# Kernel optimization log

Hardware: AMD Instinct MI355X
Metric: run time of the kernel (lower is better)

Reference implementation:

```python
import jax, jax.numpy as jnp
import numpy as np

# static config (matches torch module instantiation)
B, D, NH, HD = 2, 256, 8, 32
NL, NP, DFF = 1, 4, 1024
SHAPES = [(180, 180)]          # (H, W) per level; 180*180 = 32400
STARTS = [0]
LSRC = 32400
N_DET, N_SEG = 200, 100        # SEG_QUERY_NUM=100 -> num_seg_query=300
LQ = N_DET + N_SEG


def _lin(key, dout, din, scale=None):
    scale = scale if scale is not None else 1.0 / np.sqrt(din)
    k1, k2 = jax.random.split(key)
    return (jax.random.normal(k1, (dout, din), jnp.float32) * scale,
            jax.random.normal(k2, (dout,), jnp.float32) * 0.01)


def setup_inputs() -> dict:
    key = jax.random.key(0)
    ks = iter(jax.random.split(key, 64))
    inp = {
        'query': jax.random.normal(next(ks), (B, LQ, D), jnp.float32),
        'query_pos': jax.random.normal(next(ks), (B, LQ, D), jnp.float32),
        'src': jax.random.normal(next(ks), (B, LSRC, D), jnp.float32),
        'pos': jax.random.normal(next(ks), (B, LSRC, D), jnp.float32),
        'reference_points': jax.random.uniform(next(ks), (B, LSRC + LQ, NL, 2), jnp.float32),
        'spatial_shapes': jnp.array(SHAPES, jnp.int32),
        'level_start_index': jnp.array(STARTS, jnp.int32),
    }
    # two MSDeformAttn instances (self_attn = sa_*, cross_attn = ca_*)
    for pre in ('sa', 'ca'):
        inp[pre + '_Wv'], inp[pre + '_bv'] = _lin(next(ks), D, D)
        inp[pre + '_Woff'], inp[pre + '_boff'] = _lin(next(ks), NH * NL * NP * 2, D, scale=0.01)
        inp[pre + '_Waw'], inp[pre + '_baw'] = _lin(next(ks), NH * NL * NP, D, scale=0.01)
        inp[pre + '_Wout'], inp[pre + '_bout'] = _lin(next(ks), D, D)
    for nm in ('norm1', 'norm2', 'normq', 'qa_norm', 'norm3'):
        inp[nm + '_g'] = jnp.ones((D,), jnp.float32)
        inp[nm + '_b'] = jnp.zeros((D,), jnp.float32)
    inp['ffn1_W1'], inp['ffn1_b1'] = _lin(next(ks), DFF, D)
    inp['ffn1_W2'], inp['ffn1_b2'] = _lin(next(ks), D, DFF)
    inp['ffn3_W1'], inp['ffn3_b1'] = _lin(next(ks), DFF, D)
    inp['ffn3_W2'], inp['ffn3_b2'] = _lin(next(ks), D, DFF)
    # TCSLayer: proj(d->2d) then gate1/gate2 (d->d), sigmoid gates
    inp['tcs_Wp'], inp['tcs_bp'] = _lin(next(ks), 2 * D, D)
    inp['tcs_Wg1'], inp['tcs_bg1'] = _lin(next(ks), D, D)
    inp['tcs_Wg2'], inp['tcs_bg2'] = _lin(next(ks), D, D)
    # query self-attention (nn.MultiheadAttention): packed in_proj [3D, D]
    inp['qa_Win'], inp['qa_bin'] = _lin(next(ks), 3 * D, D)
    inp['qa_Wout'], inp['qa_bout'] = _lin(next(ks), D, D)
    return inp


def ln(x, g, b, eps=1e-5):
    m = x.mean(-1, keepdims=True)
    v = ((x - m) ** 2).mean(-1, keepdims=True)
    return (x - m) * jax.lax.rsqrt(v + eps) * g + b


def msda(q, ref, src_v, Wv, bv, Woff, boff, Waw, baw, Wout, bout):
    """MSDeformAttn: value proj -> learned offsets/weights -> bilinear sample -> out proj.
    q [B,Lq,D], ref [B,Lq,NL,2] in [0,1], src_v [B,Lin,D]."""
    Bq, Lq, _ = q.shape
    Lin = src_v.shape[1]
    value = (src_v @ Wv.T + bv).reshape(Bq, Lin, NH, HD).transpose(0, 2, 1, 3)  # [B,NH,Lin,HD]
    off = (q @ Woff.T + boff).reshape(Bq, Lq, NH, NL, NP, 2)
    aw = jax.nn.softmax((q @ Waw.T + baw).reshape(Bq, Lq, NH, NL * NP), -1)
    aw = aw.reshape(Bq, Lq, NH, NL, NP)
    norm = jnp.array([[w, h] for (h, w) in SHAPES], q.dtype)  # [NL,2] = (W,H)
    loc = ref[:, :, None, :, None, :] + off / norm[None, None, None, :, None, :]
    out = jnp.zeros((Bq, NH, Lq, HD), q.dtype)
    for l, (h, w) in enumerate(SHAPES):
        s = STARTS[l]
        v_l = value[:, :, s:s + h * w, :]
        # grid_sample align_corners=False: pixel = loc*size - 0.5, zero padding
        x = loc[:, :, :, l, :, 0] * w - 0.5  # [B,Lq,NH,NP]
        y = loc[:, :, :, l, :, 1] * h - 0.5
        x0 = jnp.floor(x); y0 = jnp.floor(y)
        lx = x - x0; ly = y - y0
        x0i = x0.astype(jnp.int32); y0i = y0.astype(jnp.int32)
        samp = jnp.zeros((Bq, NH, Lq, NP, HD), q.dtype)
        for dy, dx, wgt in ((0, 0, (1 - lx) * (1 - ly)), (0, 1, lx * (1 - ly)),
                            (1, 0, (1 - lx) * ly), (1, 1, lx * ly)):
            xi = x0i + dx; yi = y0i + dy
            valid = ((xi >= 0) & (xi < w) & (yi >= 0) & (yi < h)).astype(q.dtype)
            idx = jnp.clip(yi, 0, h - 1) * w + jnp.clip(xi, 0, w - 1)  # [B,Lq,NH,NP]
            idx_t = idx.transpose(0, 2, 1, 3).reshape(Bq, NH, Lq * NP)
            g = jnp.take_along_axis(v_l, idx_t[..., None], axis=2).reshape(Bq, NH, Lq, NP, HD)
            samp = samp + g * (wgt * valid).transpose(0, 2, 1, 3)[..., None]
        out = out + jnp.einsum('bhqpd,bqhp->bhqd', samp, aw[:, :, :, l, :])
    out = out.transpose(0, 2, 1, 3).reshape(Bq, Lq, NH * HD)
    return out @ Wout.T + bout


def mha(x, pos, Win, bin_, Wout, bout):
    qk = x + pos
    q = (qk @ Win[:D].T + bin_[:D]).reshape(*x.shape[:2], NH, HD)
    k = (qk @ Win[D:2 * D].T + bin_[D:2 * D]).reshape(*x.shape[:2], NH, HD)
    v = (x @ Win[2 * D:].T + bin_[2 * D:]).reshape(*x.shape[:2], NH, HD)
    attn = jax.nn.softmax(jnp.einsum('bqhd,bkhd->bhqk', q, k) / np.sqrt(HD), -1)
    o = jnp.einsum('bhqk,bkhd->bqhd', attn, v).reshape(*x.shape[:2], D)
    return o @ Wout.T + bout


def reference(query, query_pos, src, pos, reference_points, spatial_shapes, level_start_index,
              sa_Wv, sa_bv, sa_Woff, sa_boff, sa_Waw, sa_baw, sa_Wout, sa_bout,
              ca_Wv, ca_bv, ca_Woff, ca_boff, ca_Waw, ca_baw, ca_Wout, ca_bout,
              norm1_g, norm1_b, norm2_g, norm2_b, normq_g, normq_b,
              qa_norm_g, qa_norm_b, norm3_g, norm3_b,
              ffn1_W1, ffn1_b1, ffn1_W2, ffn1_b2,
              ffn3_W1, ffn3_b1, ffn3_W2, ffn3_b2,
              tcs_Wp, tcs_bp, tcs_Wg1, tcs_bg1, tcs_Wg2, tcs_bg2,
              qa_Win, qa_bin, qa_Wout, qa_bout):
    # deformable self-attn over BEV tokens
    src2 = msda(src + pos, reference_points[:, :LSRC], src,
                sa_Wv, sa_bv, sa_Woff, sa_boff, sa_Waw, sa_baw, sa_Wout, sa_bout)
    src = ln(src + src2, norm1_g, norm1_b)
    # FFN 1
    h = jax.nn.relu(src @ ffn1_W1.T + ffn1_b1) @ ffn1_W2.T + ffn1_b2
    src = ln(src + h, norm2_g, norm2_b)
    # TCS gating (USE_SIGMOID_GATE, not SPLIT_GATE, no OCC)
    gd, gs = jnp.split(jax.nn.gelu(src @ tcs_Wp.T + tcs_bp, approximate=False), 2, axis=-1)
    gate_det = jax.nn.sigmoid(gd @ tcs_Wg1.T + tcs_bg1)
    gate_seg = jax.nn.sigmoid(gs @ tcs_Wg2.T + tcs_bg2)
    # gated deformable cross-attn (shared cross_attn weights)
    q_det = msda(query[:, :N_DET] + query_pos[:, :N_DET],
                 reference_points[:, LSRC:LSRC + N_DET], src * gate_det,
                 ca_Wv, ca_bv, ca_Woff, ca_boff, ca_Waw, ca_baw, ca_Wout, ca_bout)
    q_seg = msda(query[:, N_DET:LQ] + query_pos[:, N_DET:LQ],
                 reference_points[:, LSRC + N_DET:LSRC + LQ], src * gate_seg,
                 ca_Wv, ca_bv, ca_Woff, ca_boff, ca_Waw, ca_baw, ca_Wout, ca_bout)
    query2 = jnp.concatenate([q_det, q_seg], 1)
    query = ln(query + query2, normq_g, normq_b)
    # query self-attention (post-norm)
    query = ln(query + mha(query, query_pos, qa_Win, qa_bin, qa_Wout, qa_bout),
               qa_norm_g, qa_norm_b)
    # FFN 3
    h3 = jax.nn.relu(query @ ffn3_W1.T + ffn3_b1) @ ffn3_W2.T + ffn3_b2
    query = ln(query + h3, norm3_g, norm3_b)
    return (query, src, gate_det, gate_seg)
```

## Files before the change

kernel.cpp:

```cpp
#include <hip/hip_runtime.h>
#include <hip/hip_bf16.h>
#include <cmath>

using bf16 = __hip_bfloat16;
typedef __bf16 bf16x8 __attribute__((ext_vector_type(8)));
typedef __bf16 bf16x4 __attribute__((ext_vector_type(4)));
typedef float f32x4 __attribute__((ext_vector_type(4)));

constexpr int D = 256;
constexpr int LSRC = 32400;
constexpr int NB = 2;
constexpr int LQ = 300;
constexpr int NDET = 200;
constexpr int MS = NB * LSRC;
constexpr int MQ = NB * LQ;
constexpr int RP_STRIDE = LSRC + LQ;
constexpr float IMGW = 180.f, IMGH = 180.f;
constexpr int IW = 180, IH = 180;

constexpr long long OFF_Q  = 0;
constexpr long long OFF_S  = (long long)MQ * D;
constexpr long long OFF_GD = OFF_S + (long long)MS * D;
constexpr long long OFF_GS = OFF_GD + (long long)MS * D;

__device__ inline void gload16(const void* g, void* l) {
  __builtin_amdgcn_global_load_lds(
      (const __attribute__((address_space(1))) void*)g,
      (__attribute__((address_space(3))) void*)l, 16, 0, 0);
}

__device__ inline int xcd_swz(int b, int nwg) {
  int q = nwg >> 3, r = nwg & 7;
  int xcd = b & 7, i = b >> 3;
  return (xcd < r ? xcd * (q + 1) : r * (q + 1) + (xcd - r) * q) + i;
}

__global__ void detect_kernel(const void* g, int* flag) {
  *flag = (*(const unsigned*)g == 0x3F803F80u) ? 1 : 0;
}

struct CvtEnt { const void* src; void* dst; int n; int f32out; };
struct CvtBatch { CvtEnt e[48]; int blk0[49]; int cnt; };

__global__ __launch_bounds__(256) void cvt_batch_kernel(CvtBatch cb, const int* __restrict__ flag) {
  int bid = blockIdx.x;
  int i = 0;
  for (int j = 1; j < cb.cnt; ++j) if (cb.blk0[j] <= bid) i = j;
  const CvtEnt en = cb.e[i];
  int idx = (bid - cb.blk0[i]) * 2048 + threadIdx.x * 8;
  if (idx >= en.n) return;
  const bool isb = (*flag != 0);
  if (en.f32out) {
    float v[8];
    if (isb) {
      bf16x8 x = *(const bf16x8*)((const __bf16*)en.src + idx);
#pragma unroll
      for (int j = 0; j < 8; ++j) v[j] = (float)x[j];
    } else {
      const float* s = (const float*)en.src + idx;
#pragma unroll
      for (int j = 0; j < 8; ++j) v[j] = s[j];
    }
    float* o = (float*)en.dst + idx;
#pragma unroll
    for (int j = 0; j < 8; ++j) o[j] = v[j];
  } else {
    if (isb) {
      uint4 x = *(const uint4*)((const char*)en.src + (size_t)idx * 2);
      *(uint4*)((char*)en.dst + (size_t)idx * 2) = x;
    } else {
      const float* s = (const float*)en.src + idx;
      bf16x8 o;
#pragma unroll
      for (int j = 0; j < 8; ++j) o[j] = (__bf16)s[j];
      *(bf16x8*)((__bf16*)en.dst + idx) = o;
    }
  }
}

__global__ __launch_bounds__(256) void cvt_add(const void* __restrict__ a, const void* __restrict__ b,
                                               const int* __restrict__ flag,
                                               bf16* __restrict__ a_b, bf16* __restrict__ b_b,
                                               bf16* __restrict__ sum, int n8) {
  int i = blockIdx.x * 256 + threadIdx.x;
  if (i >= n8) return;
  const bool isb = (*flag != 0);
  float va[8], vb[8];
  bf16x8 ab, bb;
  if (isb) {
    ab = *(const bf16x8*)((const __bf16*)a + (size_t)i * 8);
    bb = *(const bf16x8*)((const __bf16*)b + (size_t)i * 8);
#pragma unroll
    for (int j = 0; j < 8; ++j) { va[j] = (float)ab[j]; vb[j] = (float)bb[j]; }
  } else {
    const float* pa = (const float*)a + (size_t)i * 8;
    const float* pb = (const float*)b + (size_t)i * 8;
#pragma unroll
    for (int j = 0; j < 8; ++j) { va[j] = pa[j]; vb[j] = pb[j]; ab[j] = (__bf16)va[j]; bb[j] = (__bf16)vb[j]; }
  }
  bf16x8 sb;
#pragma unroll
  for (int j = 0; j < 8; ++j) sb[j] = (__bf16)(va[j] + vb[j]);
  if (a_b) *(bf16x8*)((__bf16*)a_b + (size_t)i * 8) = ab;
  if (b_b) *(bf16x8*)((__bf16*)b_b + (size_t)i * 8) = bb;
  *(bf16x8*)((__bf16*)sum + (size_t)i * 8) = sb;
}

__global__ __launch_bounds__(256) void add8(const bf16* __restrict__ a, const bf16* __restrict__ b,
                                            bf16* __restrict__ o, int n8) {
  int i = blockIdx.x * 256 + threadIdx.x;
  if (i >= n8) return;
  bf16x8 va = *(const bf16x8*)((const __bf16*)a + (size_t)i * 8);
  bf16x8 vb = *(const bf16x8*)((const __bf16*)b + (size_t)i * 8);
  bf16x8 vo;
#pragma unroll
  for (int j = 0; j < 8; ++j) vo[j] = (__bf16)((float)va[j] + (float)vb[j]);
  *(bf16x8*)((__bf16*)o + (size_t)i * 8) = vo;
}

template<int ACT, int OUTB, int RESM>
__global__ __launch_bounds__(256) void gemm_bt(
    const bf16* __restrict__ A, int lda,
    const bf16* __restrict__ Wt,
    const bf16* __restrict__ bias,
    const void* __restrict__ res,
    void* __restrict__ out, int ldo,
    int M, int N, int K)
{
  __shared__ __bf16 As[2][64 * 32];
  __shared__ __bf16 Bs[2][64 * 32];
  const int gy = gridDim.y;
  const int nwg = gridDim.x * gy;
  const int t = xcd_swz(blockIdx.y * gridDim.x + blockIdx.x, nwg);
  const int m0 = (t / gy) * 64;
  const int n0 = (t % gy) * 64;
  const int tid = threadIdx.x;
  const int lane = tid & 63, wid = tid >> 6;
  const int wm = (wid >> 1) * 32, wn = (wid & 1) * 32;
  f32x4 acc[2][2] = {};
  const int lr = tid >> 2;
  const int lc = (tid & 3) * 8;
  const bf16* Ap = A + (size_t)(m0 + lr) * lda + lc;
  const bf16* Wp = Wt + (size_t)(n0 + lr) * K + lc;
  const int fr = lane & 15, ks = (lane >> 4) * 8;

  for (int k0 = 0; k0 < K; k0 += 64) {
    __syncthreads();
#pragma unroll
    for (int kk = 0; kk < 2; ++kk) {
      const int kc = k0 + kk * 32;
      gload16((const __bf16*)Ap + kc, &As[kk][8 * tid]);
      gload16((const __bf16*)Wp + kc, &Bs[kk][8 * tid]);
    }
    __syncthreads();
#pragma unroll
    for (int kk = 0; kk < 2; ++kk) {
      bf16x8 a0 = *(const bf16x8*)&As[kk][(wm + fr) * 32 + ks];
      bf16x8 a1 = *(const bf16x8*)&As[kk][(wm + 16 + fr) * 32 + ks];
      bf16x8 b0 = *(const bf16x8*)&Bs[kk][(wn + fr) * 32 + ks];
      bf16x8 b1 = *(const bf16x8*)&Bs[kk][(wn + 16 + fr) * 32 + ks];
      acc[0][0] = __builtin_amdgcn_mfma_f32_16x16x32_bf16(a0, b0, acc[0][0], 0, 0, 0);
      acc[0][1] = __builtin_amdgcn_mfma_f32_16x16x32_bf16(a0, b1, acc[0][1], 0, 0, 0);
      acc[1][0] = __builtin_amdgcn_mfma_f32_16x16x32_bf16(a1, b0, acc[1][0], 0, 0, 0);
      acc[1][1] = __builtin_amdgcn_mfma_f32_16x16x32_bf16(a1, b1, acc[1][1], 0, 0, 0);
    }
  }

  const int rq = (lane >> 4) * 4;
#pragma unroll
  for (int fm = 0; fm < 2; ++fm)
#pragma unroll
  for (int fn = 0; fn < 2; ++fn) {
    int ncol = n0 + wn + fn * 16 + fr;
    if (ncol >= N) continue;
    float bvs = (float)bias[ncol];
#pragma unroll
    for (int i = 0; i < 4; ++i) {
      int mrow = m0 + wm + fm * 16 + rq + i;
      if (mrow >= M) continue;
      float v = acc[fm][fn][i] + bvs;
      if (RESM == 1) v += (float)((const bf16*)res)[(size_t)mrow * ldo + ncol];
      else if (RESM == 2) v += ((const float*)res)[(size_t)mrow * ldo + ncol];
      if (ACT == 1) v = fmaxf(v, 0.f);
      else if (ACT == 2) v = 0.5f * v * (1.f + erff(v * 0.7071067811865476f));
      else if (ACT == 3) v = 1.f / (1.f + __expf(-v));
      if (OUTB) ((bf16*)out)[(size_t)mrow * ldo + ncol] = (bf16)v;
      else ((float*)out)[(size_t)mrow * ldo + ncol] = v;
    }
  }
}

template<int ACT, int OUTB, int RESM, int EMIT>
__global__ __launch_bounds__(256) void gemm128(
    const bf16* __restrict__ A, int lda,
    const bf16* __restrict__ Wt,
    const bf16* __restrict__ bias,
    const void* __restrict__ res,
    void* __restrict__ out, int ldo,
    int M, int N, int K,
    const int* __restrict__ flagp, void* __restrict__ ob, long long eoff)
{
  __shared__ __bf16 As[2][128 * 32];
  __shared__ __bf16 Bs[2][128 * 32];
  const int gy = gridDim.y;
  const int nwg = gridDim.x * gy;
  const int t = xcd_swz(blockIdx.y * gridDim.x + blockIdx.x, nwg);
  const int m0 = (t / gy) * 128;
  const int n0 = (t % gy) * 128;
  const int tid = threadIdx.x;
  const int lane = tid & 63, wid = tid >> 6;
  const int wr = (wid >> 1) * 64, wc = (wid & 1) * 64;
  const int fr = lane & 15, ks = (lane >> 4) * 8;
  f32x4 acc[4][4] = {};

  const int srow = tid >> 2;
  const int scol = (tid & 3) * 8;
  const bf16* Ap0 = A + (size_t)(m0 + srow) * lda + scol;
  const bf16* Ap1 = A + (size_t)(m0 + 64 + srow) * lda + scol;
  const bf16* Bp0 = Wt + (size_t)(n0 + srow) * K + scol;
  const bf16* Bp1 = Wt + (size_t)(n0 + 64 + srow) * K + scol;

  for (int k0 = 0; k0 < K; k0 += 64) {
    __syncthreads();
#pragma unroll
    for (int kk = 0; kk < 2; ++kk) {
      const int kc = k0 + kk * 32;
      gload16((const __bf16*)Ap0 + kc, &As[kk][8 * tid]);
      gload16((const __bf16*)Ap1 + kc, &As[kk][64 * 32 + 8 * tid]);
      gload16((const __bf16*)Bp0 + kc, &Bs[kk][8 * tid]);
      gload16((const __bf16*)Bp1 + kc, &Bs[kk][64 * 32 + 8 * tid]);
    }
    __syncthreads();
#pragma unroll
    for (int kk = 0; kk < 2; ++kk) {
      bf16x8 af[4], bfv[4];
#pragma unroll
      for (int m = 0; m < 4; ++m) af[m]  = *(const bf16x8*)&As[kk][(wr + m * 16 + fr) * 32 + ks];
#pragma unroll
      for (int n = 0; n < 4; ++n) bfv[n] = *(const bf16x8*)&Bs[kk][(wc + n * 16 + fr) * 32 + ks];
#pragma unroll
      for (int m = 0; m < 4; ++m)
#pragma unroll
        for (int n = 0; n < 4; ++n)
          acc[m][n] = __builtin_amdgcn_mfma_f32_16x16x32_bf16(af[m], bfv[n], acc[m][n], 0, 0, 0);
    }
  }

  const bool isb = EMIT ? (*flagp != 0) : false;
  const int rq = (lane >> 4) * 4;
#pragma unroll
  for (int m = 0; m < 4; ++m) {
    const int mb = m0 + wr + m * 16 + rq;
#pragma unroll
    for (int n = 0; n < 4; ++n) {
      const int ncol = n0 + wc + n * 16 + fr;
      const float bvs = (float)bias[ncol];
#pragma unroll
      for (int i = 0; i < 4; ++i) {
        const int mrow = mb + i;
        if (mrow >= M) continue;
        float v = acc[m][n][i] + bvs;
        if (RESM == 1) v += (float)((const bf16*)res)[(size_t)mrow * ldo + ncol];
        else if (RESM == 2) v += ((const float*)res)[(size_t)mrow * ldo + ncol];
        if (ACT == 1) v = fmaxf(v, 0.f);
        else if (ACT == 2) v = 0.5f * v * (1.f + erff(v * 0.7071067811865476f));
        else if (ACT == 3) v = 1.f / (1.f + __expf(-v));
        if (OUTB) ((bf16*)out)[(size_t)mrow * ldo + ncol] = (bf16)v;
        else ((float*)out)[(size_t)mrow * ldo + ncol] = v;
        if (EMIT) {
          long long eo = eoff + (long long)mrow * ldo + ncol;
          if (isb) ((__bf16*)ob)[eo] = (__bf16)v;
          else ((float*)ob)[eo] = v;
        }
      }
    }
  }
}

__global__ __launch_bounds__(256) void gemm_gated(
    const bf16* __restrict__ S, const bf16* __restrict__ G, int lda,
    const bf16* __restrict__ Wt,
    const bf16* __restrict__ bias,
    bf16* __restrict__ out, int ldo,
    int M, int N, int K)
{
  __shared__ __bf16 As[2][128 * 32];
  __shared__ __bf16 Bs[2][128 * 32];
  const int gy = gridDim.y;
  const int nwg = gridDim.x * gy;
  const int t = xcd_swz(blockIdx.y * gridDim.x + blockIdx.x, nwg);
  const int m0 = (t / gy) * 128;
  const int n0 = (t % gy) * 128;
  const int tid = threadIdx.x;
  const int lane = tid & 63, wid = tid >> 6;
  const int wr = (wid >> 1) * 64, wc = (wid & 1) * 64;
  const int fr = lane & 15, ks = (lane >> 4) * 8;
  f32x4 acc[4][4] = {};

  const int srow = tid >> 2;
  const int scol = (tid & 3) * 8;
  const bf16* Sp0 = S + (size_t)(m0 + srow) * lda + scol;
  const bf16* Sp1 = S + (size_t)(m0 + 64 + srow) * lda + scol;
  const bf16* Gp0 = G + (size_t)(m0 + srow) * lda + scol;
  const bf16* Gp1 = G + (size_t)(m0 + 64 + srow) * lda + scol;
  const bf16* Bp0 = Wt + (size_t)(n0 + srow) * K + scol;
  const bf16* Bp1 = Wt + (size_t)(n0 + 64 + srow) * K + scol;

  for (int k0 = 0; k0 < K; k0 += 64) {
    bf16x8 a0[2], a1[2];
#pragma unroll
    for (int kk = 0; kk < 2; ++kk) {
      const int kc = k0 + kk * 32;
      bf16x8 s0 = *(const bf16x8*)((const __bf16*)Sp0 + kc);
      bf16x8 g0 = *(const bf16x8*)((const __bf16*)Gp0 + kc);
      bf16x8 s1 = *(const bf16x8*)((const __bf16*)Sp1 + kc);
      bf16x8 g1 = *(const bf16x8*)((const __bf16*)Gp1 + kc);
#pragma unroll
      for (int j = 0; j < 8; ++j) {
        a0[kk][j] = (__bf16)((float)s0[j] * (float)g0[j]);
        a1[kk][j] = (__bf16)((float)s1[j] * (float)g1[j]);
      }
    }
    __syncthreads();
#pragma unroll
    for (int kk = 0; kk < 2; ++kk) {
      const int kc = k0 + kk * 32;
      *(bf16x8*)&As[kk][8 * tid] = a0[kk];
      *(bf16x8*)&As[kk][64 * 32 + 8 * tid] = a1[kk];
      gload16((const __bf16*)Bp0 + kc, &Bs[kk][8 * tid]);
      gload16((const __bf16*)Bp1 + kc, &Bs[kk][64 * 32 + 8 * tid]);
    }
    __syncthreads();
#pragma unroll
    for (int kk = 0; kk < 2; ++kk) {
      bf16x8 af[4], bfv[4];
#pragma unroll
      for (int m = 0; m < 4; ++m) af[m]  = *(const bf16x8*)&As[kk][(wr + m * 16 + fr) * 32 + ks];
#pragma unroll
      for (int n = 0; n < 4; ++n) bfv[n] = *(const bf16x8*)&Bs[kk][(wc + n * 16 + fr) * 32 + ks];
#pragma unroll
      for (int m = 0; m < 4; ++m)
#pragma unroll
        for (int n = 0; n < 4; ++n)
          acc[m][n] = __builtin_amdgcn_mfma_f32_16x16x32_bf16(af[m], bfv[n], acc[m][n], 0, 0, 0);
    }
  }

  const int rq = (lane >> 4) * 4;
#pragma unroll
  for (int m = 0; m < 4; ++m) {
    const int mb = m0 + wr + m * 16 + rq;
#pragma unroll
    for (int n = 0; n < 4; ++n) {
      const int ncol = n0 + wc + n * 16 + fr;
      const float bvs = (float)bias[ncol];
#pragma unroll
      for (int i = 0; i < 4; ++i) {
        const int mrow = mb + i;
        if (mrow >= M) continue;
        out[(size_t)mrow * ldo + ncol] = (bf16)(acc[m][n][i] + bvs);
      }
    }
  }
}

template<int RESM, int EMIT, int OUTF>
__global__ __launch_bounds__(256) void gemm_ln(
    const bf16* __restrict__ A, int lda,
    const bf16* __restrict__ Wt,
    const bf16* __restrict__ bias,
    const void* __restrict__ res,
    const bf16* __restrict__ g, const bf16* __restrict__ b,
    bf16* __restrict__ outb, float* __restrict__ outf,
    int M, int K,
    const int* __restrict__ flagp, void* __restrict__ ob, long long eoff)
{
  __shared__ __bf16 As[2][64 * 32];
  __shared__ __bf16 Bs[2][256 * 32];
  __shared__ float redS[4][64], redQ[4][64];
  const int m0 = blockIdx.x * 64;
  const int tid = threadIdx.x, lane = tid & 63, wid = tid >> 6;
  const int wc = wid * 64;
  const int fr = lane & 15, ks = (lane >> 4) * 8;
  f32x4 acc[4][4] = {};
  const int srow = tid >> 2, scol = (tid & 3) * 8;
  const bf16* Ap = A + (size_t)(m0 + srow) * lda + scol;
  const bf16* Bp = Wt + (size_t)srow * K + scol;

  for (int k0 = 0; k0 < K; k0 += 64) {
    __syncthreads();
#pragma unroll
    for (int kk = 0; kk < 2; ++kk) {
      const int kc = k0 + kk * 32;
      gload16((const __bf16*)Ap + kc, &As[kk][8 * tid]);
#pragma unroll
      for (int j = 0; j < 4; ++j)
        gload16((const __bf16*)(Bp + (size_t)j * 64 * K) + kc, &Bs[kk][j * 64 * 32 + 8 * tid]);
    }
    __syncthreads();
#pragma unroll
    for (int kk = 0; kk < 2; ++kk) {
      bf16x8 af[4], bfv[4];
#pragma unroll
      for (int m = 0; m < 4; ++m) af[m]  = *(const bf16x8*)&As[kk][(m * 16 + fr) * 32 + ks];
#pragma unroll
      for (int n = 0; n < 4; ++n) bfv[n] = *(const bf16x8*)&Bs[kk][(wc + n * 16 + fr) * 32 + ks];
#pragma unroll
      for (int m = 0; m < 4; ++m)
#pragma unroll
        for (int n = 0; n < 4; ++n)
          acc[m][n] = __builtin_amdgcn_mfma_f32_16x16x32_bf16(af[m], bfv[n], acc[m][n], 0, 0, 0);
    }
  }

  const int rq = (lane >> 4) * 4;
  float bvals[4], gvals[4], bb2[4];
#pragma unroll
  for (int n = 0; n < 4; ++n) {
    bvals[n] = (float)bias[wc + n * 16 + fr];
    gvals[n] = (float)g[wc + n * 16 + fr];
    bb2[n]   = (float)b[wc + n * 16 + fr];
  }
#pragma unroll
  for (int m = 0; m < 4; ++m)
#pragma unroll
  for (int i = 0; i < 4; ++i) {
    const int mrow = m0 + m * 16 + rq + i;
#pragma unroll
    for (int n = 0; n < 4; ++n) {
      float r;
      if (RESM == 1) r = (float)((const bf16*)res)[(size_t)mrow * 256 + wc + n * 16 + fr];
      else           r = ((const float*)res)[(size_t)mrow * 256 + wc + n * 16 + fr];
      acc[m][n][i] += bvals[n] + r;
    }
    float s = acc[m][0][i] + acc[m][1][i] + acc[m][2][i] + acc[m][3][i];
    float q = acc[m][0][i] * acc[m][0][i] + acc[m][1][i] * acc[m][1][i]
            + acc[m][2][i] * acc[m][2][i] + acc[m][3][i] * acc[m][3][i];
#pragma unroll
    for (int off = 1; off <= 8; off <<= 1) {
      s += __shfl_xor(s, off);
      q += __shfl_xor(q, off);
    }
    if (fr == 0) { redS[wid][m * 16 + rq + i] = s; redQ[wid][m * 16 + rq + i] = q; }
  }
  __syncthreads();
  const bool isb = EMIT ? (*flagp != 0) : false;
#pragma unroll
  for (int m = 0; m < 4; ++m)
#pragma unroll
  for (int i = 0; i < 4; ++i) {
    const int rl = m * 16 + rq + i;
    const int mrow = m0 + rl;
    if (mrow >= M) continue;
    float ts = redS[0][rl] + redS[1][rl] + redS[2][rl] + redS[3][rl];
    float tq = redQ[0][rl] + redQ[1][rl] + redQ[2][rl] + redQ[3][rl];
    float mean = ts * (1.f / 256.f);
    float var = tq * (1.f / 256.f) - mean * mean;
    float rstd = rsqrtf(var + 1e-5f);
#pragma unroll
    for (int n = 0; n < 4; ++n) {
      const int col = wc + n * 16 + fr;
      float y = (acc[m][n][i] - mean) * rstd * gvals[n] + bb2[n];
      if (outb) outb[(size_t)mrow * 256 + col] = (bf16)y;
      if (OUTF) outf[(size_t)mrow * 256 + col] = y;
      if (EMIT) {
        long long eo = eoff + (long long)mrow * 256 + col;
        if (isb) ((__bf16*)ob)[eo] = (__bf16)y;
        else ((float*)ob)[eo] = y;
      }
    }
  }
}

__global__ __launch_bounds__(256) void msda_sample4(
    const float* __restrict__ oa,
    const float* __restrict__ rpf, int rp_base, int qi0, int qcnt4, int lqrow,
    const bf16* __restrict__ val, bf16* __restrict__ out, int swz) {
  int blk = blockIdx.x;
  if (swz) blk = xcd_swz(blk, gridDim.x);
  int b = blk / qcnt4;
  int wid = threadIdx.x >> 6, lane = threadIdx.x & 63;
  int qi = qi0 + (blk % qcnt4) * 4 + wid;
  size_t row = (size_t)b * lqrow + qi;
  int h = lane >> 3, d0 = (lane & 7) * 4;
  const __bf16* vb = (const __bf16*)val + (size_t)b * LSRC * 256 + h * 32 + d0;
  float rx = rpf[((size_t)b * RP_STRIDE + rp_base + qi) * 2 + 0];
  float ry = rpf[((size_t)b * RP_STRIDE + rp_base + qi) * 2 + 1];
  const float* offp = oa + row * 96 + h * 8;
  const float* awp  = oa + row * 96 + 64 + h * 4;
  float a0 = awp[0], a1 = awp[1], a2 = awp[2], a3 = awp[3];
  float mx = fmaxf(fmaxf(a0, a1), fmaxf(a2, a3));
  float e0 = __expf(a0 - mx), e1 = __expf(a1 - mx), e2 = __expf(a2 - mx), e3 = __expf(a3 - mx);
  float rs = 1.f / (e0 + e1 + e2 + e3);
  float aws[4] = { e0 * rs, e1 * rs, e2 * rs, e3 * rs };
  float o0 = 0.f, o1 = 0.f, o2 = 0.f, o3 = 0.f;
#pragma unroll
  for (int p = 0; p < 4; ++p) {
    float x = rx * IMGW + offp[p * 2 + 0] - 0.5f;
    float y = ry * IMGH + offp[p * 2 + 1] - 0.5f;
    float x0f = floorf(x), y0f = floorf(y);
    float lx = x - x0f, ly = y - y0f;
    int x0 = (int)x0f, y0 = (int)y0f;
#pragma unroll
    for (int dy = 0; dy < 2; ++dy)
#pragma unroll
    for (int dx = 0; dx < 2; ++dx) {
      int xi = x0 + dx, yi = y0 + dy;
      if (xi >= 0 && xi < IW && yi >= 0 && yi < IH) {
        float wgt = aws[p] * (dx ? lx : 1.f - lx) * (dy ? ly : 1.f - ly);
        bf16x4 gv = *(const bf16x4*)(vb + (size_t)(yi * IW + xi) * 256);
        o0 += wgt * (float)gv[0]; o1 += wgt * (float)gv[1];
        o2 += wgt * (float)gv[2]; o3 += wgt * (float)gv[3];
      }
    }
  }
  bf16x4 ov;
  ov[0] = (__bf16)o0; ov[1] = (__bf16)o1; ov[2] = (__bf16)o2; ov[3] = (__bf16)o3;
  *(bf16x4*)((__bf16*)out + row * 256 + h * 32 + d0) = ov;
}

__global__ __launch_bounds__(256) void mha_attn(
    const float* __restrict__ qk,
    const float* __restrict__ v,
    bf16* __restrict__ o) {
  __shared__ float probs[4][304];
  int bh = blockIdx.x / 75;
  int j  = blockIdx.x % 75;
  int b = bh >> 3, h = bh & 7;
  int wid = threadIdx.x >> 6, lane = threadIdx.x & 63;
  const float scale = 0.17677669529663687f;
  int q = j * 4 + wid;
  const float* qv = qk + ((size_t)(b * 300 + q)) * 512 + h * 32;
  float p[5];
  float mx = -1e30f;
#pragma unroll
  for (int s5 = 0; s5 < 5; ++s5) {
    int k = lane + 64 * s5;
    float sacc = -1e30f;
    if (k < 300) {
      const float* kv = qk + ((size_t)(b * 300 + k)) * 512 + 256 + h * 32;
      float sd = 0.f;
#pragma unroll
      for (int dd = 0; dd < 32; ++dd) sd += qv[dd] * kv[dd];
      sacc = sd * scale;
    }
    p[s5] = sacc;
    mx = fmaxf(mx, sacc);
  }
#pragma unroll
  for (int off = 32; off; off >>= 1) mx = fmaxf(mx, __shfl_xor(mx, off));
  float ssum = 0.f;
#pragma unroll
  for (int s5 = 0; s5 < 5; ++s5) {
    p[s5] = (p[s5] > -1e29f) ? __expf(p[s5] - mx) : 0.f;
    ssum += p[s5];
  }
#pragma unroll
  for (int off = 32; off; off >>= 1) ssum += __shfl_xor(ssum, off);
  float rinv = 1.f / ssum;
#pragma unroll
  for (int s5 = 0; s5 < 5; ++s5) {
    int k = lane + 64 * s5;
    if (k < 300) probs[wid][k] = p[s5] * rinv;
  }
  __syncthreads();
  {
    int d = lane & 31, half = lane >> 5;
    float acc = 0.f;
    for (int k = half * 150; k < half * 150 + 150; ++k)
      acc += probs[wid][k] * v[((size_t)(b * 300 + k)) * 256 + h * 32 + d];
    acc += __shfl_xor(acc, 32);
    if (lane < 32) o[((size_t)(b * 300 + q)) * 256 + h * 32 + d] = (bf16)acc;
  }
}

extern "C" void kernel_launch(void* const* d_in, const int* in_sizes, int n_in,
                              void* d_out, int out_size, void* d_ws, size_t ws_size,
                              hipStream_t stream) {
  (void)n_in; (void)out_size; (void)ws_size;
  const size_t SZ = (size_t)MS * D * sizeof(bf16);

  char* w = (char*)d_ws;
  auto carve = [&](size_t bytes) { char* p = w; w += (bytes + 255) & ~(size_t)255; return p; };

  int*   flag = (int*)carve(256);
  float* rp_f = (float*)carve((size_t)NB * RP_STRIDE * 2 * 4);

  bf16* wb[51] = {};
  bf16* wcat_s = nullptr; bf16* bcat_s = nullptr;
  bf16* wcat_q = nullptr; bf16* bcat_q = nullptr;
  for (int i = 7; i <= 50; ++i) {
    if (i == 9)       { wcat_s = (bf16*)carve((size_t)96 * 256 * 2); wb[9]  = wcat_s; }
    else if (i == 10) { bcat_s = (bf16*)carve(96 * 2);               wb[10] = bcat_s; }
    else if (i == 11) { wb[11] = wcat_s + 64 * 256; }
    else if (i == 12) { wb[12] = bcat_s + 64; }
    else if (i == 17) { wcat_q = (bf16*)carve((size_t)96 * 256 * 2); wb[17] = wcat_q; }
    else if (i == 18) { bcat_q = (bf16*)carve(96 * 2);               wb[18] = bcat_q; }
    else if (i == 19) { wb[19] = wcat_q + 64 * 256; }
    else if (i == 20) { wb[20] = bcat_q + 64; }
    else wb[i] = (bf16*)carve((size_t)in_sizes[i] * 2);
  }

  bf16* query_b     = (bf16*)carve((size_t)MQ * D * 2);
  bf16* query_pos_b = (bf16*)carve((size_t)MQ * D * 2);
  bf16* qx_q        = (bf16*)carve((size_t)MQ * D * 2);
  bf16* att_q       = (bf16*)carve((size_t)MQ * D * 2);
  bf16* q_x         = (bf16*)carve((size_t)MQ * D * 2);
  bf16* qpx         = (bf16*)carve((size_t)MQ * D * 2);
  bf16* mha_o       = (bf16*)carve((size_t)MQ * D * 2);
  bf16* lnq_b       = (bf16*)carve((size_t)MQ * D * 2);
  bf16* qh          = (bf16*)carve((size_t)MQ * 1024 * 2);
  float* qoffawb    = (float*)carve((size_t)MQ * 96 * 4);
  float* q_res      = (float*)carve((size_t)MQ * D * 4);
  float* qk_f       = (float*)carve((size_t)MQ * 512 * 4);
  float* v_f        = (float*)carve((size_t)MQ * D * 4);

  char* A = carve(SZ);
  char* B = carve(SZ);
  char* C = carve(SZ);
  char* Dd = carve(SZ);
  char* E = carve(SZ);
  carve(512 * 1024);

  const bf16* query     = (const bf16*)d_in[0];
  const bf16* query_pos = (const bf16*)d_in[1];
  const bf16* src       = (const bf16*)d_in[2];
  const bf16* pos       = (const bf16*)d_in[3];

  dim3 blk(256);
  const int GS64  = (MS + 63) / 64;
  const int GQ64  = (MQ + 63) / 64;
  const int G128  = (MS + 127) / 128;
  const int G128h = (MS / 2 + 127) / 128;

  detect_kernel<<<1, 1, 0, stream>>>(d_in[23], flag);
  {
    CvtBatch cb{};
    int nb = 0, cnt = 0;
    auto addcvt = [&](const void* s, void* dst, int n, int f32o) {
      cb.e[cnt] = { s, dst, n, f32o };
      cb.blk0[cnt] = nb;
      nb += (n + 2047) / 2048;
      ++cnt;
    };
    addcvt(d_in[4], rp_f, in_sizes[4], 1);
    for (int i = 7; i <= 50; ++i) addcvt(d_in[i], wb[i], in_sizes[i], 0);
    cb.cnt = cnt;
    cvt_batch_kernel<<<nb, blk, 0, stream>>>(cb, flag);
  }
  bf16* src_b = (bf16*)A;
  bf16* qx    = (bf16*)C;
  cvt_add<<<MS * D / 8 / 256, blk, 0, stream>>>(src, pos, flag, src_b, nullptr, qx, MS * D / 8);
  cvt_add<<<MQ * D / 8 / 256, blk, 0, stream>>>(query, query_pos, flag, query_b, query_pos_b, qx_q, MQ * D / 8);

  float* offawb = (float*)B;
  bf16*  val    = (bf16*)Dd;
  gemm_bt<0,0,0><<<dim3(GS64,2), blk, 0, stream>>>(qx, 256, wb[9], wb[10], nullptr, offawb, 96, MS, 96, 256);
  gemm128<0,1,0,0><<<dim3(G128,2), blk, 0, stream>>>(src_b, 256, wb[7], wb[8], nullptr, val, 256, MS, 256, 256, nullptr, nullptr, 0);
  bf16* samp = (bf16*)C;
  msda_sample4<<<NB * (LSRC / 4), blk, 0, stream>>>(offawb, rp_f, 0, 0, LSRC / 4, LSRC, val, samp, 1);
  bf16* lnx = (bf16*)C;
  gemm_ln<1,0,0><<<GS64, blk, 0, stream>>>(samp, 256, wb[13], wb[14], src_b, wb[23], wb[24],
                                           lnx, nullptr, MS, 256, nullptr, nullptr, 0);

  bf16* srcout = (bf16*)A;
  {
    const int CH = MS / 2;
    const int GC128 = (CH + 127) / 128;
    const int GC64  = (CH + 63) / 64;
    bf16* hid = (bf16*)Dd;
    for (int c = 0; c < 2; ++c) {
      size_t ro = (size_t)c * CH * 256;
      gemm128<1,1,0,0><<<dim3(GC128,8), blk, 0, stream>>>(lnx + ro, 256, wb[33], wb[34], nullptr, hid, 1024, CH, 1024, 256, nullptr, nullptr, 0);
      gemm_ln<1,1,0><<<GC64, blk, 0, stream>>>(hid, 1024, wb[35], wb[36], lnx + ro, wb[25], wb[26],
                                               srcout + ro, nullptr, CH, 1024, flag, d_out, OFF_S + (long long)ro);
    }
  }

  bf16* gdt = (bf16*)B;
  bf16* gst = (bf16*)E;
  {
    const int CH = MS / 2;
    bf16* proj = (bf16*)C;
    for (int c = 0; c < 2; ++c) {
      size_t ro = (size_t)c * CH * 256;
      gemm128<2,1,0,0><<<dim3(G128h,4), blk, 0, stream>>>(srcout + ro, 256, wb[41], wb[42], nullptr, proj, 512, CH, 512, 256, nullptr, nullptr, 0);
      gemm128<3,1,0,1><<<dim3(G128h,2), blk, 0, stream>>>(proj,       512, wb[43], wb[44], nullptr, gdt + ro, 256, CH, 256, 256, flag, d_out, OFF_GD + (long long)ro);
      gemm128<3,1,0,1><<<dim3(G128h,2), blk, 0, stream>>>(proj + 256, 512, wb[45], wb[46], nullptr, gst + ro, 256, CH, 256, 256, flag, d_out, OFF_GS + (long long)ro);
    }
  }

  gemm_bt<0,0,0><<<dim3(GQ64,2), blk, 0, stream>>>(qx_q, 256, wb[17], wb[18], nullptr, qoffawb, 96, MQ, 96, 256);

  gemm_gated<<<dim3(G128,2), blk, 0, stream>>>(srcout, gdt, 256, wb[15], wb[16], val, 256, MS, 256, 256);
  msda_sample4<<<NB * (NDET / 4), blk, 0, stream>>>(qoffawb, rp_f, LSRC, 0, NDET / 4, LQ, val, att_q, 0);
  gemm_gated<<<dim3(G128,2), blk, 0, stream>>>(srcout, gst, 256, wb[15], wb[16], val, 256, MS, 256, 256);
  msda_sample4<<<NB * ((LQ - NDET) / 4), blk, 0, stream>>>(qoffawb, rp_f, LSRC, NDET, (LQ - NDET) / 4, LQ, val, att_q, 0);

  gemm_ln<1,0,1><<<GQ64, blk, 0, stream>>>(att_q, 256, wb[21], wb[22], query_b, wb[27], wb[28],
                                           q_x, q_res, MQ, 256, nullptr, nullptr, 0);

  add8<<<MQ * D / 8 / 256, blk, 0, stream>>>(q_x, query_pos_b, qpx, MQ * D / 8);
  gemm_bt<0,0,0><<<dim3(GQ64,8), blk, 0, stream>>>(qpx, 256, wb[47], wb[48], nullptr, qk_f, 512, MQ, 512, 256);
  gemm_bt<0,0,0><<<dim3(GQ64,4), blk, 0, stream>>>(q_x, 256, wb[47] + (size_t)512 * 256, wb[48] + 512, nullptr, v_f, 256, MQ, 256, 256);
  mha_attn<<<NB * 8 * 75, blk, 0, stream>>>(qk_f, v_f, mha_o);
  gemm_ln<2,0,1><<<GQ64, blk, 0, stream>>>(mha_o, 256, wb[49], wb[50], q_res, wb[29], wb[30],
                                           q_x, q_res, MQ, 256, nullptr, nullptr, 0);

  gemm_bt<1,1,0><<<dim3(GQ64,16), blk, 0, stream>>>(q_x, 256, wb[37], wb[38], nullptr, qh, 1024, MQ, 1024, 256);
  gemm_ln<2,1,0><<<GQ64, blk, 0, stream>>>(qh, 1024, wb[39], wb[40], q_res, wb[31], wb[32],
                                           lnq_b, nullptr, MQ, 1024, flag, d_out, OFF_Q);
}
```

Before: 759.2 us.

## Fuse input conversion and adds into GEMM loads, merge gated cross-attn passes

Removes the large src+pos convert/add pass and instead reads the raw inputs (fp32 or bf16) directly inside the offset/attention GEMM, value GEMM and residual of the LayerNorm GEMM. The two gated value projections now run as one launch over a z-dimension into separate buffers, so the det and seg sampling run as a single kernel. The gate projection loops are unchunked into full-size launches, and the query+pos add before the MHA projection is folded into the GEMM's A-load. This saves a full-size intermediate write and read and several launches, at the cost of extra buffer space and redundant fp32 loads, since both GEMMs now read src separately.

```diff
diff --git a/kernel.cpp b/kernel.cpp
--- a/kernel.cpp
+++ b/kernel.cpp
@@ -33,6 +33,31 @@
   int q = nwg >> 3, r = nwg & 7;
   int xcd = b & 7, i = b >> 3;
   return (xcd < r ? xcd * (q + 1) : r * (q + 1) + (xcd - r) * q) + i;
+}
+
+__device__ inline bf16x8 ld8_dyn(const void* p, size_t off, bool isb) {
+  if (isb) return *(const bf16x8*)((const __bf16*)p + off);
+  bf16x8 r;
+  const float* f = (const float*)p + off;
+#pragma unroll
+  for (int j = 0; j < 8; ++j) r[j] = (__bf16)f[j];
+  return r;
+}
+
+__device__ inline bf16x8 ld8_add_dyn(const void* a, const void* b, size_t off, bool isb) {
+  bf16x8 r;
+  if (isb) {
+    bf16x8 x = *(const bf16x8*)((const __bf16*)a + off);
+    bf16x8 y = *(const bf16x8*)((const __bf16*)b + off);
+#pragma unroll
+    for (int j = 0; j < 8; ++j) r[j] = (__bf16)((float)x[j] + (float)y[j]);
+  } else {
+    const float* fa = (const float*)a + off;
+    const float* fb = (const float*)b + off;
+#pragma unroll
+    for (int j = 0; j < 8; ++j) r[j] = (__bf16)(fa[j] + fb[j]);
+  }
+  return r;
 }
 
 __global__ void detect_kernel(const void* g, int* flag) {
@@ -104,18 +129,6 @@
   if (a_b) *(bf16x8*)((__bf16*)a_b + (size_t)i * 8) = ab;
   if (b_b) *(bf16x8*)((__bf16*)b_b + (size_t)i * 8) = bb;
   *(bf16x8*)((__bf16*)sum + (size_t)i * 8) = sb;
-}
-
-__global__ __launch_bounds__(256) void add8(const bf16* __restrict__ a, const bf16* __restrict__ b,
-                                            bf16* __restrict__ o, int n8) {
-  int i = blockIdx.x * 256 + threadIdx.x;
-  if (i >= n8) return;
-  bf16x8 va = *(const bf16x8*)((const __bf16*)a + (size_t)i * 8);
-  bf16x8 vb = *(const bf16x8*)((const __bf16*)b + (size_t)i * 8);
-  bf16x8 vo;
-#pragma unroll
-  for (int j = 0; j < 8; ++j) vo[j] = (__bf16)((float)va[j] + (float)vb[j]);
-  *(bf16x8*)((__bf16*)o + (size_t)i * 8) = vo;
 }
 
 template<int ACT, int OUTB, int RESM>
@@ -190,6 +203,74 @@
   }
 }
 
+template<int ADYN>
+__global__ __launch_bounds__(256) void gemm_bt_add(
+    const void* __restrict__ A1, const void* __restrict__ A2, int lda,
+    const bf16* __restrict__ Wt, const bf16* __restrict__ bias,
+    float* __restrict__ out, int ldo, int M, int N, int K,
+    const int* __restrict__ flagp)
+{
+  __shared__ __bf16 As[2][64 * 32];
+  __shared__ __bf16 Bs[2][64 * 32];
+  const int gy = gridDim.y;
+  const int nwg = gridDim.x * gy;
+  const int t = xcd_swz(blockIdx.y * gridDim.x + blockIdx.x, nwg);
+  const int m0 = (t / gy) * 64;
+  const int n0 = (t % gy) * 64;
+  const int tid = threadIdx.x;
+  const int lane = tid & 63, wid = tid >> 6;
+  const int wm = (wid >> 1) * 32, wn = (wid & 1) * 32;
+  f32x4 acc[2][2] = {};
+  const int lr = tid >> 2;
+  const int lc = (tid & 3) * 8;
+  const int ar = min(m0 + lr, M - 1);
+  const size_t abase = (size_t)ar * lda + lc;
+  const bf16* Wp = Wt + (size_t)(n0 + lr) * K + lc;
+  const bool isb = ADYN ? (*flagp != 0) : true;
+  const int fr = lane & 15, ks = (lane >> 4) * 8;
+
+  for (int k0 = 0; k0 < K; k0 += 64) {
+    bf16x8 av[2];
+#pragma unroll
+    for (int kk = 0; kk < 2; ++kk)
+      av[kk] = ld8_add_dyn(A1, A2, abase + k0 + kk * 32, isb);
+    __syncthreads();
+#pragma unroll
+    for (int kk = 0; kk < 2; ++kk) {
+      *(bf16x8*)&As[kk][8 * tid] = av[kk];
+      gload16((const __bf16*)Wp + k0 + kk * 32, &Bs[kk][8 * tid]);
+    }
+    __syncthreads();
+#pragma unroll
+    for (int kk = 0; kk < 2; ++kk) {
+      bf16x8 a0 = *(const bf16x8*)&As[kk][(wm + fr) * 32 + ks];
+      bf16x8 a1 = *(const bf16x8*)&As[kk][(wm + 16 + fr) * 32 + ks];
+      bf16x8 b0 = *(const bf16x8*)&Bs[kk][(wn + fr) * 32 + ks];
+      bf16x8 b1 = *(const bf16x8*)&Bs[kk][(wn + 16 + fr) * 32 + ks];
+      acc[0][0] = __builtin_amdgcn_mfma_f32_16x16x32_bf16(a0, b0, acc[0][0], 0, 0, 0);
+      acc[0][1] = __builtin_amdgcn_mfma_f32_16x16x32_bf16(a0, b1, acc[0][1], 0, 0, 0);
+      acc[1][0] = __builtin_amdgcn_mfma_f32_16x16x32_bf16(a1, b0, acc[1][0], 0, 0, 0);
+      acc[1][1] = __builtin_amdgcn_mfma_f32_16x16x32_bf16(a1, b1, acc[1][1], 0, 0, 0);
+    }
+  }
+
+  const int rq = (lane >> 4) * 4;
+#pragma unroll
+  for (int fm = 0; fm < 2; ++fm)
+#pragma unroll
+  for (int fn = 0; fn < 2; ++fn) {
+    int ncol = n0 + wn + fn * 16 + fr;
+    if (ncol >= N) continue;
+    float bvs = (float)bias[ncol];
+#pragma unroll
+    for (int i = 0; i < 4; ++i) {
+      int mrow = m0 + wm + fm * 16 + rq + i;
+      if (mrow >= M) continue;
+      out[(size_t)mrow * ldo + ncol] = acc[fm][fn][i] + bvs;
+    }
+  }
+}
+
 template<int ACT, int OUTB, int RESM, int EMIT>
 __global__ __launch_bounds__(256) void gemm128(
     const bf16* __restrict__ A, int lda,
@@ -277,15 +358,18 @@
   }
 }
 
-__global__ __launch_bounds__(256) void gemm_gated(
-    const bf16* __restrict__ S, const bf16* __restrict__ G, int lda,
-    const bf16* __restrict__ Wt,
-    const bf16* __restrict__ bias,
-    bf16* __restrict__ out, int ldo,
-    int M, int N, int K)
+template<int OP, int SDYN>
+__global__ __launch_bounds__(256) void gemm128_rs(
+    const void* __restrict__ S, const bf16* __restrict__ G0, const bf16* __restrict__ G1,
+    int lda,
+    const bf16* __restrict__ Wt, const bf16* __restrict__ bias,
+    bf16* __restrict__ out0, bf16* __restrict__ out1, int ldo,
+    int M, int N, int K, const int* __restrict__ flagp)
 {
   __shared__ __bf16 As[2][128 * 32];
   __shared__ __bf16 Bs[2][128 * 32];
+  const bf16* G = blockIdx.z ? G1 : G0;
+  bf16* out = blockIdx.z ? out1 : out0;
   const int gy = gridDim.y;
   const int nwg = gridDim.x * gy;
   const int t = xcd_swz(blockIdx.y * gridDim.x + blockIdx.x, nwg);
@@ -299,32 +383,38 @@
 
   const int srow = tid >> 2;
   const int scol = (tid & 3) * 8;
-  const bf16* Sp0 = S + (size_t)(m0 + srow) * lda + scol;
-  const bf16* Sp1 = S + (size_t)(m0 + 64 + srow) * lda + scol;
-  const bf16* Gp0 = G + (size_t)(m0 + srow) * lda + scol;
-  const bf16* Gp1 = G + (size_t)(m0 + 64 + srow) * lda + scol;
+  const int r0 = min(m0 + srow, M - 1);
+  const int r1 = min(m0 + 64 + srow, M - 1);
+  const size_t s0off = (size_t)r0 * lda + scol;
+  const size_t s1off = (size_t)r1 * lda + scol;
   const bf16* Bp0 = Wt + (size_t)(n0 + srow) * K + scol;
   const bf16* Bp1 = Wt + (size_t)(n0 + 64 + srow) * K + scol;
+  const bool isb = SDYN ? (*flagp != 0) : true;
 
   for (int k0 = 0; k0 < K; k0 += 64) {
     bf16x8 a0[2], a1[2];
 #pragma unroll
     for (int kk = 0; kk < 2; ++kk) {
-      const int kc = k0 + kk * 32;
-      bf16x8 s0 = *(const bf16x8*)((const __bf16*)Sp0 + kc);
-      bf16x8 g0 = *(const bf16x8*)((const __bf16*)Gp0 + kc);
-      bf16x8 s1 = *(const bf16x8*)((const __bf16*)Sp1 + kc);
-      bf16x8 g1 = *(const bf16x8*)((const __bf16*)Gp1 + kc);
-#pragma unroll
-      for (int j = 0; j < 8; ++j) {
-        a0[kk][j] = (__bf16)((float)s0[j] * (float)g0[j]);
-        a1[kk][j] = (__bf16)((float)s1[j] * (float)g1[j]);
+      const int kc = kk * 32 + k0;
+      bf16x8 s0 = ld8_dyn(S, s0off + kc, isb);
+      bf16x8 s1 = ld8_dyn(S, s1off + kc, isb);
+      if (OP == 1) {
+        bf16x8 g0 = *(const bf16x8*)((const __bf16*)G + s0off + kc);
+        bf16x8 g1 = *(const bf16x8*)((const __bf16*)G + s1off + kc);
+#pragma unroll
+        for (int j = 0; j < 8; ++j) {
+          a0[kk][j] = (__bf16)((float)s0[j] * (float)g0[j]);
+          a1[kk][j] = (__bf16)((float)s1[j] * (float)g1[j]);
+        }
+      } else {
+        a0[kk] = s0;
+        a1[kk] = s1;
       }
     }
     __syncthreads();
 #pragma unroll
     for (int kk = 0; kk < 2; ++kk) {
-      const int kc = k0 + kk * 32;
+      const int kc = kk * 32 + k0;
       *(bf16x8*)&As[kk][8 * tid] = a0[kk];
       *(bf16x8*)&As[kk][64 * 32 + 8 * tid] = a1[kk];
       gload16((const __bf16*)Bp0 + kc, &Bs[kk][8 * tid]);
@@ -414,6 +504,7 @@
   }
 
   const int rq = (lane >> 4) * 4;
+  const bool fb = (EMIT || RESM == 3) ? (*flagp != 0) : false;
   float bvals[4], gvals[4], bb2[4];
 #pragma unroll
   for (int n = 0; n < 4; ++n) {
@@ -426,11 +517,14 @@
 #pragma unroll
   for (int i = 0; i < 4; ++i) {
     const int mrow = m0 + m * 16 + rq + i;
+    const int rr = mrow < M ? mrow : M - 1;
 #pragma unroll
     for (int n = 0; n < 4; ++n) {
+      const size_t ri = (size_t)rr * 256 + wc + n * 16 + fr;
       float r;
-      if (RESM == 1) r = (float)((const bf16*)res)[(size_t)mrow * 256 + wc + n * 16 + fr];
-      else           r = ((const float*)res)[(size_t)mrow * 256 + wc + n * 16 + fr];
+      if (RESM == 1) r = (float)((const bf16*)res)[ri];
+      else if (RESM == 2) r = ((const float*)res)[ri];
+      else r = fb ? (float)((const bf16*)res)[ri] : ((const float*)res)[ri];
       acc[m][n][i] += bvals[n] + r;
     }
     float s = acc[m][0][i] + acc[m][1][i] + acc[m][2][i] + acc[m][3][i];
@@ -444,7 +538,6 @@
     if (fr == 0) { redS[wid][m * 16 + rq + i] = s; redQ[wid][m * 16 + rq + i] = q; }
   }
   __syncthreads();
-  const bool isb = EMIT ? (*flagp != 0) : false;
 #pragma unroll
   for (int m = 0; m < 4; ++m)
 #pragma unroll
@@ -465,7 +558,7 @@
       if (OUTF) outf[(size_t)mrow * 256 + col] = y;
       if (EMIT) {
         long long eo = eoff + (long long)mrow * 256 + col;
-        if (isb) ((__bf16*)ob)[eo] = (__bf16)y;
+        if (fb) ((__bf16*)ob)[eo] = (__bf16)y;
         else ((float*)ob)[eo] = y;
       }
     }
@@ -474,15 +567,17 @@
 
 __global__ __launch_bounds__(256) void msda_sample4(
     const float* __restrict__ oa,
-    const float* __restrict__ rpf, int rp_base, int qi0, int qcnt4, int lqrow,
-    const bf16* __restrict__ val, bf16* __restrict__ out, int swz) {
+    const float* __restrict__ rpf, int rp_base, int qcnt4, int lqrow, int split,
+    const bf16* __restrict__ valA, const bf16* __restrict__ valB,
+    bf16* __restrict__ out, int swz) {
   int blk = blockIdx.x;
   if (swz) blk = xcd_swz(blk, gridDim.x);
   int b = blk / qcnt4;
   int wid = threadIdx.x >> 6, lane = threadIdx.x & 63;
-  int qi = qi0 + (blk % qcnt4) * 4 + wid;
+  int qi = (blk % qcnt4) * 4 + wid;
   size_t row = (size_t)b * lqrow + qi;
   int h = lane >> 3, d0 = (lane & 7) * 4;
+  const bf16* val = (qi < split) ? valA : valB;
   const __bf16* vb = (const __bf16*)val + (size_t)b * LSRC * 256 + h * 32 + d0;
   float rx = rpf[((size_t)b * RP_STRIDE + rp_base + qi) * 2 + 0];
   float ry = rpf[((size_t)b * RP_STRIDE + rp_base + qi) * 2 + 1];
@@ -606,7 +701,6 @@
   bf16* qx_q        = (bf16*)carve((size_t)MQ * D * 2);
   bf16* att_q       = (bf16*)carve((size_t)MQ * D * 2);
   bf16* q_x         = (bf16*)carve((size_t)MQ * D * 2);
-  bf16* qpx         = (bf16*)carve((size_t)MQ * D * 2);
   bf16* mha_o       = (bf16*)carve((size_t)MQ * D * 2);
   bf16* lnq_b       = (bf16*)carve((size_t)MQ * D * 2);
   bf16* qh          = (bf16*)carve((size_t)MQ * 1024 * 2);
@@ -624,14 +718,13 @@
 
   const bf16* query     = (const bf16*)d_in[0];
   const bf16* query_pos = (const bf16*)d_in[1];
-  const bf16* src       = (const bf16*)d_in[2];
-  const bf16* pos       = (const bf16*)d_in[3];
+  const void* src       = d_in[2];
+  const void* pos       = d_in[3];
 
   dim3 blk(256);
   const int GS64  = (MS + 63) / 64;
   const int GQ64  = (MQ + 63) / 64;
   const int G128  = (MS + 127) / 128;
-  const int G128h = (MS / 2 + 127) / 128;
 
   detect_kernel<<<1, 1, 0, stream>>>(d_in[23], flag);
   {
@@ -648,20 +741,17 @@
     cb.cnt = cnt;
     cvt_batch_kernel<<<nb, blk, 0, stream>>>(cb, flag);
   }
-  bf16* src_b = (bf16*)A;
-  bf16* qx    = (bf16*)C;
-  cvt_add<<<MS * D / 8 / 256, blk, 0, stream>>>(src, pos, flag, src_b, nullptr, qx, MS * D / 8);
   cvt_add<<<MQ * D / 8 / 256, blk, 0, stream>>>(query, query_pos, flag, query_b, query_pos_b, qx_q, MQ * D / 8);
 
   float* offawb = (float*)B;
   bf16*  val    = (bf16*)Dd;
-  gemm_bt<0,0,0><<<dim3(GS64,2), blk, 0, stream>>>(qx, 256, wb[9], wb[10], nullptr, offawb, 96, MS, 96, 256);
-  gemm128<0,1,0,0><<<dim3(G128,2), blk, 0, stream>>>(src_b, 256, wb[7], wb[8], nullptr, val, 256, MS, 256, 256, nullptr, nullptr, 0);
+  gemm_bt_add<1><<<dim3(GS64,2), blk, 0, stream>>>(src, pos, 256, wb[9], wb[10], offawb, 96, MS, 96, 256, flag);
+  gemm128_rs<0,1><<<dim3(G128,2,1), blk, 0, stream>>>(src, nullptr, nullptr, 256, wb[7], wb[8], val, nullptr, 256, MS, 256, 256, flag);
   bf16* samp = (bf16*)C;
-  msda_sample4<<<NB * (LSRC / 4), blk, 0, stream>>>(offawb, rp_f, 0, 0, LSRC / 4, LSRC, val, samp, 1);
+  msda_sample4<<<NB * (LSRC / 4), blk, 0, stream>>>(offawb, rp_f, 0, LSRC / 4, LSRC, 1 << 30, val, val, samp, 1);
   bf16* lnx = (bf16*)C;
-  gemm_ln<1,0,0><<<GS64, blk, 0, stream>>>(samp, 256, wb[13], wb[14], src_b, wb[23], wb[24],
-                                           lnx, nullptr, MS, 256, nullptr, nullptr, 0);
+  gemm_ln<3,0,0><<<GS64, blk, 0, stream>>>(samp, 256, wb[13], wb[14], src, wb[23], wb[24],
+                                           lnx, nullptr, MS, 256, flag, nullptr, 0);
 
   bf16* srcout = (bf16*)A;
   {
@@ -677,31 +767,25 @@
     }
   }
 
-  bf16* gdt = (bf16*)B;
-  bf16* gst = (bf16*)E;
-  {
-    const int CH = MS / 2;
-    bf16* proj = (bf16*)C;
-    for (int c = 0; c < 2; ++c) {
-      size_t ro = (size_t)c * CH * 256;
-      gemm128<2,1,0,0><<<dim3(G128h,4), blk, 0, stream>>>(srcout + ro, 256, wb[41], wb[42], nullptr, proj, 512, CH, 512, 256, nullptr, nullptr, 0);
-      gemm128<3,1,0,1><<<dim3(G128h,2), blk, 0, stream>>>(proj,       512, wb[43], wb[44], nullptr, gdt + ro, 256, CH, 256, 256, flag, d_out, OFF_GD + (long long)ro);
-      gemm128<3,1,0,1><<<dim3(G128h,2), blk, 0, stream>>>(proj + 256, 512, wb[45], wb[46], nullptr, gst + ro, 256, CH, 256, 256, flag, d_out, OFF_GS + (long long)ro);
-    }
-  }
+  bf16* proj = (bf16*)Dd;
+  bf16* gdt  = (bf16*)B;
+  bf16* gst  = (bf16*)C;
+  gemm128<2,1,0,0><<<dim3(G128,4), blk, 0, stream>>>(srcout, 256, wb[41], wb[42], nullptr, proj, 512, MS, 512, 256, nullptr, nullptr, 0);
+  gemm128<3,1,0,1><<<dim3(G128,2), blk, 0, stream>>>(proj,       512, wb[43], wb[44], nullptr, gdt, 256, MS, 256, 256, flag, d_out, OFF_GD);
+  gemm128<3,1,0,1><<<dim3(G128,2), blk, 0, stream>>>(proj + 256, 512, wb[45], wb[46], nullptr, gst, 256, MS, 256, 256, flag, d_out, OFF_GS);
 
   gemm_bt<0,0,0><<<dim3(GQ64,2), blk, 0, stream>>>(qx_q, 256, wb[17], wb[18], nullptr, qoffawb, 96, MQ, 96, 256);
 
-  gemm_gated<<<dim3(G128,2), blk, 0, stream>>>(srcout, gdt, 256, wb[15], wb[16], val, 256, MS, 256, 256);
-  msda_sample4<<<NB * (NDET / 4), blk, 0, stream>>>(qoffawb, rp_f, LSRC, 0, NDET / 4, LQ, val, att_q, 0);
-  gemm_gated<<<dim3(G128,2), blk, 0, stream>>>(srcout, gst, 256, wb[15], wb[16], val, 256, MS, 256, 256);
-  msda_sample4<<<NB * ((LQ - NDET) / 4), blk, 0, stream>>>(qoffawb, rp_f, LSRC, NDET, (LQ - NDET) / 4, LQ, val, att_q, 0);
+  bf16* val_det = (bf16*)Dd;
+  bf16* val_seg = (bf16*)E;
+  gemm128_rs<1,0><<<dim3(G128,2,2), blk, 0, stream>>>(srcout, gdt, gst, 256, wb[15], wb[16],
+                                                      val_det, val_seg, 256, MS, 256, 256, nullptr);
+  msda_sample4<<<NB * (LQ / 4), blk, 0, stream>>>(qoffawb, rp_f, LSRC, LQ / 4, LQ, NDET, val_det, val_seg, att_q, 0);
 
   gemm_ln<1,0,1><<<GQ64, blk, 0, stream>>>(att_q, 256, wb[21], wb[22], query_b, wb[27], wb[28],
                                            q_x, q_res, MQ, 256, nullptr, nullptr, 0);
 
-  add8<<<MQ * D / 8 / 256, blk, 0, stream>>>(q_x, query_pos_b, qpx, MQ * D / 8);
-  gemm_bt<0,0,0><<<dim3(GQ64,8), blk, 0, stream>>>(qpx, 256, wb[47], wb[48], nullptr, qk_f, 512, MQ, 512, 256);
+  gemm_bt_add<0><<<dim3(GQ64,8), blk, 0, stream>>>(q_x, query_pos_b, 256, wb[47], wb[48], qk_f, 512, MQ, 512, 256, flag);
   gemm_bt<0,0,0><<<dim3(GQ64,4), blk, 0, stream>>>(q_x, 256, wb[47] + (size_t)512 * 256, wb[48] + 512, nullptr, v_f, 256, MQ, 256, 256);
   mha_attn<<<NB * 8 * 75, blk, 0, stream>>>(qk_f, v_f, mha_o);
   gemm_ln<2,0,1><<<GQ64, blk, 0, stream>>>(mha_o, 256, wb[49], wb[50], q_res, wb[29], wb[30],
```

Result: faster. 741.6 us (-2.3%).
